# Kernel optimization log

Measured on AMD Instinct MI355X. Metric: run time of the kernel, lower is better.

Reference implementation:

```python
import jax, jax.numpy as jnp
import numpy as np

B, N, D = 8, 4096, 256


def setup_inputs() -> dict:
    key = jax.random.key(0)
    ks = jax.random.split(key, 4)
    seq = jax.random.normal(ks[0], (B, N, D), dtype=jnp.float32)
    W_fts = jax.random.normal(ks[1], (D, D), dtype=jnp.float32) * (1.0 / np.sqrt(D))
    w_f1 = jax.random.normal(ks[2], (D, 1), dtype=jnp.float32) * (1.0 / np.sqrt(D))
    b_f1 = jnp.zeros((1,), dtype=jnp.float32)
    w_f2 = jax.random.normal(ks[3], (D, 1), dtype=jnp.float32) * (1.0 / np.sqrt(D))
    b_f2 = jnp.zeros((1,), dtype=jnp.float32)
    bias = jnp.zeros((1,), dtype=jnp.float32)
    return {"seq": seq, "W_fts": W_fts, "w_f1": w_f1, "b_f1": b_f1,
            "w_f2": w_f2, "b_f2": b_f2, "bias": bias}


def reference(seq, W_fts, w_f1, b_f1, w_f2, b_f2, bias):
    # seq: [B, N, D]
    seq_fts = jnp.einsum('bnd,de->bne', seq, W_fts)          # values, [B, N, D]
    f_1 = seq @ w_f1 + b_f1                                   # [B, N, 1]
    f_2 = seq @ w_f2 + b_f2                                   # [B, N, 1]
    logits = f_1 + jnp.swapaxes(f_2, 1, 2)                    # broadcast add -> [B, N, N]
    coefs = jax.nn.softmax(jax.nn.leaky_relu(logits, negative_slope=0.01), axis=-1)
    vals = jnp.einsum('bnm,bmd->bnd', coefs, seq_fts)         # [B, N, D]
    ret = vals + bias
    return jax.nn.relu(ret)
```

## Files before the change

kernel.cpp:

```cpp
#include <hip/hip_runtime.h>
#include <hip/hip_bf16.h>
#include <math.h>

#define B 8
#define N 4096
#define D 256
#define BN (B*N)
#define NSUP 64
#define NS1 65
#define NR1 4097

typedef __attribute__((ext_vector_type(8))) short bf16x8;
typedef __attribute__((ext_vector_type(4))) float f32x4;

#define GLD16(src, dst) __builtin_amdgcn_global_load_lds( \
    (const __attribute__((address_space(1))) void*)(src), \
    (__attribute__((address_space(3))) void*)(dst), 16, 0, 0)

__device__ __forceinline__ ushort bf16_hi(float x) {
  __hip_bfloat16 h = __float2bfloat16(x);
  return *(ushort*)&h;
}
__device__ __forceinline__ ushort bf16_lo(float x) {
  __hip_bfloat16 h = __float2bfloat16(x);
  float hf = __bfloat162float(h);
  __hip_bfloat16 l = __float2bfloat16(x - hf);
  return *(ushort*)&l;
}

__global__ __launch_bounds__(256) void k_f1f2w(const float* __restrict__ seq,
    const float* __restrict__ w1, const float* __restrict__ b1,
    const float* __restrict__ w2, const float* __restrict__ b2,
    const float* __restrict__ W, float* __restrict__ f1, float* __restrict__ f2,
    int* __restrict__ rank, ushort* __restrict__ W3) {
  if (blockIdx.x >= BN/4) {
    int n = blockIdx.x - BN/4;
    int k = threadIdx.x;
    float x = W[(size_t)k * D + n];
    ushort hu = bf16_hi(x), lu = bf16_lo(x);
    W3[(size_t)n * 768 + k] = hu;
    W3[(size_t)n * 768 + 256 + k] = lu;
    W3[(size_t)n * 768 + 512 + k] = hu;
    return;
  }
  int wave = threadIdx.x >> 6;
  int lane = threadIdx.x & 63;
  long row = (long)blockIdx.x * 4 + wave;
  float4 v = ((const float4*)(seq + row * D))[lane];
  float4 a = ((const float4*)w1)[lane];
  float4 b = ((const float4*)w2)[lane];
  float s1 = v.x*a.x + v.y*a.y + v.z*a.z + v.w*a.w;
  float s2 = v.x*b.x + v.y*b.y + v.z*b.z + v.w*b.w;
  for (int off = 32; off; off >>= 1) {
    s1 += __shfl_xor(s1, off, 64);
    s2 += __shfl_xor(s2, off, 64);
  }
  if (lane == 0) {
    f1[row] = s1 + b1[0];
    f2[row] = s2 + b2[0];
    rank[row] = 0;
  }
}

__global__ __launch_bounds__(256) void k_rank_count(const float* __restrict__ f2,
    int* __restrict__ rank) {
  __shared__ unsigned long long skey[256];
  int b = blockIdx.z;
  int tid = threadIdx.x;
  const float* fb = f2 + (long)b * N;
  int p = blockIdx.y * 256 + tid;
  unsigned int up = __float_as_uint(fb[p]);
  up ^= (unsigned int)(((int)up >> 31) | 0x80000000);
  skey[tid] = ((unsigned long long)up << 12) | (unsigned)p;
  unsigned long long kj[4];
  int jbase = blockIdx.x * 1024;
  #pragma unroll
  for (int q = 0; q < 4; ++q) {
    int j = jbase + q * 256 + tid;
    unsigned int uj = __float_as_uint(fb[j]);
    uj ^= (unsigned int)(((int)uj >> 31) | 0x80000000);
    kj[q] = ((unsigned long long)uj << 12) | (unsigned)j;
  }
  __syncthreads();
  int c[4] = {0, 0, 0, 0};
  const ulonglong2* sk2 = (const ulonglong2*)skey;
  #pragma unroll 4
  for (int pp = 0; pp < 128; ++pp) {
    ulonglong2 kk = sk2[pp];
    #pragma unroll
    for (int q = 0; q < 4; ++q) {
      c[q] += (kk.x < kj[q]) ? 1 : 0;
      c[q] += (kk.y < kj[q]) ? 1 : 0;
    }
  }
  #pragma unroll
  for (int q = 0; q < 4; ++q)
    atomicAdd(&rank[(long)b * N + jbase + q * 256 + tid], c[q]);
}

__global__ __launch_bounds__(256) void k_scatter(const float* __restrict__ f2,
    const int* __restrict__ rank, float* __restrict__ sF2, int* __restrict__ sIdx,
    float* __restrict__ e2lo, float* __restrict__ e2hi) {
  long idx = (long)blockIdx.x * 256 + threadIdx.x;
  int b = (int)(idx >> 12);
  int j = (int)(idx & (N - 1));
  float v = f2[idx];
  int cnt = rank[idx];
  long o = (long)b * N + cnt;
  sF2[o] = v;
  sIdx[o] = j;
  e2lo[o] = expf(0.01f * v);
  e2hi[o] = expf(v);
}

__global__ __launch_bounds__(256) void k_mfma(const float* __restrict__ seq,
    const int* __restrict__ sIdx, const ushort* __restrict__ W3,
    const float* __restrict__ e2lo, const float* __restrict__ e2hi,
    float* __restrict__ Rel, float* __restrict__ Zrel,
    float* __restrict__ SupBaseLo, float* __restrict__ SupBaseHi,
    float* __restrict__ SupZlo, float* __restrict__ SupZhi) {
  __shared__ __align__(16) char smem[64 * 256 * 4];
  ushort (*As)[72] = (ushort(*)[72])smem;
  ushort (*Bs)[64] = (ushort(*)[64])(smem + 64 * 72 * 2);
  int tid = threadIdx.x;
  int wid = tid >> 6, lane = tid & 63;
  int mBase = blockIdx.x * 64;
  int b = mBase >> 12;
  int ar = tid >> 2, aq = tid & 3;
  const float* aSrc = seq + (((size_t)(b << 12)) + sIdx[mBase + ar]) * D + aq * 16;
  int lr = lane >> 3;
  int lcSw = (((lane & 7) ^ (lr & 7))) * 8;
  int wr = wid >> 1, wc = wid & 1, g = lane >> 4, r16 = lane & 15;
  int bswz = r16 & 7;

  f32x4 acc[2][8];
  #pragma unroll
  for (int m = 0; m < 2; ++m)
    #pragma unroll
    for (int n = 0; n < 8; ++n) {
      acc[m][n][0] = 0.f; acc[m][n][1] = 0.f; acc[m][n][2] = 0.f; acc[m][n][3] = 0.f;
    }

  float4 xv[4];
  #pragma unroll
  for (int i = 0; i < 4; ++i) xv[i] = *(const float4*)(aSrc + i * 4);

  for (int kt = 0; kt < 768; kt += 64) {
    ushort ou[16];
    if (kt < 512) {
      #pragma unroll
      for (int i = 0; i < 4; ++i) {
        ou[i*4+0] = bf16_hi(xv[i].x); ou[i*4+1] = bf16_hi(xv[i].y);
        ou[i*4+2] = bf16_hi(xv[i].z); ou[i*4+3] = bf16_hi(xv[i].w);
      }
    } else {
      #pragma unroll
      for (int i = 0; i < 4; ++i) {
        ou[i*4+0] = bf16_lo(xv[i].x); ou[i*4+1] = bf16_lo(xv[i].y);
        ou[i*4+2] = bf16_lo(xv[i].z); ou[i*4+3] = bf16_lo(xv[i].w);
      }
    }
    __syncthreads();
    #pragma unroll
    for (int i = 0; i < 4; ++i)
      *(ushort4*)&As[ar][aq * 16 + i * 4] =
          make_ushort4(ou[i*4+0], ou[i*4+1], ou[i*4+2], ou[i*4+3]);
    #pragma unroll
    for (int q = 0; q < 8; ++q) {
      int r0 = q * 32 + wid * 8;
      GLD16(W3 + (size_t)(r0 + lr) * 768 + kt + lcSw, &Bs[r0][0]);
    }
    if (kt < 704) {
      int nacol = (kt + 64) & 255;
      #pragma unroll
      for (int i = 0; i < 4; ++i) xv[i] = *(const float4*)(aSrc + nacol + i * 4);
    }
    __syncthreads();
    #pragma unroll
    for (int kk = 0; kk < 64; kk += 32) {
      bf16x8 av[2], bv[8];
      #pragma unroll
      for (int m = 0; m < 2; ++m)
        av[m] = *(const bf16x8*)&As[wr*32 + m*16 + r16][kk + g*8];
      int jb = (kk >> 3) + g;
      int jj = jb ^ bswz;
      #pragma unroll
      for (int n = 0; n < 8; ++n) {
        int row = wc*128 + n*16 + r16;
        bv[n] = *(const bf16x8*)((const char*)Bs + row * 128 + jj * 16);
      }
      #pragma unroll
      for (int m = 0; m < 2; ++m)
        #pragma unroll
        for (int n = 0; n < 8; ++n)
          acc[m][n] = __builtin_amdgcn_mfma_f32_16x16x32_bf16(av[m], bv[n], acc[m][n], 0, 0, 0);
    }
  }

  __syncthreads();
  float (*Vt)[256] = (float(*)[256])smem;
  int cswz = (g << 2) | ((g & 1) << 4);
  #pragma unroll
  for (int m = 0; m < 2; ++m)
    #pragma unroll
    for (int n = 0; n < 8; ++n) {
      int col = (wc*128 + n*16 + r16) ^ cswz;
      #pragma unroll
      for (int j = 0; j < 4; ++j)
        Vt[wr*32 + m*16 + g*4 + j][col] = acc[m][n][j];
    }
  __syncthreads();
  int d = tid;
  int s = (mBase >> 6) & 63;
  size_t rb = (size_t)mBase;
  float rl = 0.f, rh = 0.f;
  float* pR = Rel + ((size_t)b * NR1 + (size_t)s * 64) * 512 + 2 * d;
  #pragma unroll 8
  for (int r = 0; r < 64; ++r) {
    int gr = (r >> 2) & 3;
    int rsw = (gr << 2) | ((gr & 1) << 4);
    float wlo = e2lo[rb + r], whi = e2hi[rb + r];
    float v = Vt[r][d ^ rsw];
    float2 pr; pr.x = rl; pr.y = rh;
    *(float2*)(pR + (size_t)r * 512) = pr;
    rl += wlo * v; rh += whi * v;
  }
  SupBaseLo[((size_t)b * NS1 + s) * D + d] = rl;
  SupBaseHi[((size_t)b * NS1 + s) * D + d] = rh;
  if (tid == 0) {
    float z = 0.f;
    #pragma unroll 8
    for (int r = 0; r < 64; ++r) { Zrel[((size_t)b * NR1 + s*64 + r) * 2] = z; z += e2lo[rb + r]; }
    SupZlo[b*NS1+s] = z;
  } else if (tid == 64) {
    float z = 0.f;
    #pragma unroll 8
    for (int r = 0; r < 64; ++r) { Zrel[((size_t)b * NR1 + s*64 + r) * 2 + 1] = z; z += e2hi[rb + r]; }
    SupZhi[b*NS1+s] = z;
  }
}

__global__ __launch_bounds__(256) void k_supscan(float* __restrict__ SupBaseLo,
    float* __restrict__ SupBaseHi, float* __restrict__ SupZlo,
    float* __restrict__ SupZhi, float* __restrict__ Rel, float* __restrict__ Zrel) {
  int b = blockIdx.x, t = threadIdx.x;
  if (t < 64) {
    float4* lo = (float4*)SupBaseLo + (size_t)b * NS1 * 64 + t;
    float4* hi = (float4*)SupBaseHi + (size_t)b * NS1 * 64 + t;
    float4 rl = {0,0,0,0}, rh = {0,0,0,0};
    for (int s = 0; s < NSUP; s += 8) {
      float4 tl[8], th[8];
      #pragma unroll
      for (int u = 0; u < 8; ++u) { tl[u] = lo[(size_t)(s+u)*64]; th[u] = hi[(size_t)(s+u)*64]; }
      #pragma unroll
      for (int u = 0; u < 8; ++u) {
        lo[(size_t)(s+u)*64] = rl; hi[(size_t)(s+u)*64] = rh;
        rl.x+=tl[u].x; rl.y+=tl[u].y; rl.z+=tl[u].z; rl.w+=tl[u].w;
        rh.x+=th[u].x; rh.y+=th[u].y; rh.z+=th[u].z; rh.w+=th[u].w;
      }
    }
    lo[(size_t)NSUP*64] = rl;
    hi[(size_t)NSUP*64] = rh;
  } else if (t < 192) {
    float4 z = {0,0,0,0};
    ((float4*)(Rel + ((size_t)b * NR1 + 4096) * 512))[t - 64] = z;
  } else if (t == 192) {
    float r = 0.f;
    for (int s = 0; s < NSUP; ++s) { float x = SupZlo[b*NS1+s]; SupZlo[b*NS1+s] = r; r += x; }
    SupZlo[b*NS1+NSUP] = r;
    Zrel[((size_t)b * NR1 + 4096) * 2] = 0.f;
  } else if (t == 193) {
    float r = 0.f;
    for (int s = 0; s < NSUP; ++s) { float x = SupZhi[b*NS1+s]; SupZhi[b*NS1+s] = r; r += x; }
    SupZhi[b*NS1+NSUP] = r;
    Zrel[((size_t)b * NR1 + 4096) * 2 + 1] = 0.f;
  }
}

__global__ __launch_bounds__(256) void k_combine2(const float* __restrict__ f1,
    const float* __restrict__ sF2, const float* __restrict__ Rel,
    const float* __restrict__ SupBaseLo, const float* __restrict__ SupBaseHi,
    const float* __restrict__ SupZlo, const float* __restrict__ SupZhi,
    const float* __restrict__ Zrel,
    const float* __restrict__ bias, float* __restrict__ out) {
  int wid = threadIdx.x >> 6, lane = threadIdx.x & 63;
  size_t i = (size_t)blockIdx.x * 4 + wid;
  int b = (int)(i >> 12);
  float f1v = f1[i];
  const float* sb = sF2 + ((size_t)b << 12);
  float t = -f1v;
  int lo = 0, hi = N;
  while (lo < hi) { int mid = (lo + hi) >> 1; if (sb[mid] <= t) lo = mid + 1; else hi = mid; }
  int k = lo;
  int s = k >> 6;
  float a = expf(f1v), cc = expf(0.01f * f1v);
  const float* rrow = Rel + ((size_t)b * NR1 + k) * 512;
  float4 q0 = ((const float4*)rrow)[2*lane];
  float4 q1 = ((const float4*)rrow)[2*lane + 1];
  float4 sblo = ((const float4*)SupBaseLo)[((size_t)b * NS1 + s) * 64 + lane];
  float4 sbhi = ((const float4*)SupBaseHi)[((size_t)b * NS1 + s) * 64 + lane];
  float4 pht  = ((const float4*)SupBaseHi)[((size_t)b * NS1 + NSUP) * 64 + lane];
  float2 z2 = *(const float2*)(Zrel + ((size_t)b * NR1 + k) * 2);
  float Zlo = SupZlo[b*NS1+s] + z2.x;
  float Zhi = SupZhi[b*NS1+NSUP] - SupZhi[b*NS1+s] - z2.y;
  float Z = a * Zhi + cc * Zlo;
  float rz = 1.f / Z;
  float bs = bias[0];
  float4 o4;
  o4.x = fmaxf((a*(pht.x - sbhi.x - q0.y) + cc*(sblo.x + q0.x)) * rz + bs, 0.f);
  o4.y = fmaxf((a*(pht.y - sbhi.y - q0.w) + cc*(sblo.y + q0.z)) * rz + bs, 0.f);
  o4.z = fmaxf((a*(pht.z - sbhi.z - q1.y) + cc*(sblo.z + q1.x)) * rz + bs, 0.f);
  o4.w = fmaxf((a*(pht.w - sbhi.w - q1.w) + cc*(sblo.w + q1.z)) * rz + bs, 0.f);
  ((float4*)out)[i * 64 + lane] = o4;
}

extern "C" void kernel_launch(void* const* d_in, const int* in_sizes, int n_in,
                              void* d_out, int out_size, void* d_ws, size_t ws_size,
                              hipStream_t stream) {
  const float* seq  = (const float*)d_in[0];
  const float* Wf   = (const float*)d_in[1];
  const float* w1   = (const float*)d_in[2];
  const float* b1   = (const float*)d_in[3];
  const float* w2   = (const float*)d_in[4];
  const float* b2   = (const float*)d_in[5];
  const float* bias = (const float*)d_in[6];
  float* out = (float*)d_out;

  size_t needFloats = (size_t)7*BN + (size_t)B*NR1*512 + 2*(size_t)B*NS1*D
                    + 2*(size_t)B*NS1 + 2*(size_t)B*NR1;
  size_t need = needFloats * 4 + (size_t)256 * 768 * 2;
  if (ws_size < need) return;

  float* f1   = (float*)d_ws;
  float* f2   = f1 + BN;
  float* sF2  = f2 + BN;
  float* e2lo = sF2 + BN;
  float* e2hi = e2lo + BN;
  int* sIdx   = (int*)(e2hi + BN);
  int* rank   = sIdx + BN;
  float* Rel  = (float*)(rank + BN);
  float* SupBaseLo = Rel + (size_t)B * NR1 * 512;
  float* SupBaseHi = SupBaseLo + (size_t)B * NS1 * D;
  float* SupZlo = SupBaseHi + (size_t)B * NS1 * D;
  float* SupZhi = SupZlo + B * NS1;
  float* Zrel   = SupZhi + B * NS1;
  ushort* W3 = (ushort*)(Zrel + 2 * (size_t)B * NR1);

  k_f1f2w<<<dim3(BN/4 + 256), 256, 0, stream>>>(seq, w1, b1, w2, b2, Wf,
      f1, f2, rank, W3);
  k_rank_count<<<dim3(N/1024, N/256, B), 256, 0, stream>>>(f2, rank);
  k_scatter<<<dim3(BN/256), 256, 0, stream>>>(f2, rank, sF2, sIdx, e2lo, e2hi);
  k_mfma<<<dim3(BN/64), 256, 0, stream>>>(seq, sIdx, W3, e2lo, e2hi,
      Rel, Zrel, SupBaseLo, SupBaseHi, SupZlo, SupZhi);
  k_supscan<<<dim3(B), 256, 0, stream>>>(SupBaseLo, SupBaseHi, SupZlo, SupZhi,
      Rel, Zrel);
  k_combine2<<<dim3(BN/4), 256, 0, stream>>>(f1, sF2, Rel,
      SupBaseLo, SupBaseHi, SupZlo, SupZhi, Zrel, bias, out);
}
```

Measured before the change: 88.37 us.

## Double-buffer W3 tile in LDS and prefetch seq rows two stages ahead

The single B tile buffer in the projection MFMA kernel becomes two LDS buffers. The next W3 slice is loaded asynchronously with global_load_lds while MFMAs run on the current slice, and the bf16 hi/lo conversion of the next A chunk moves after the compute, with a second register stage prefetching seq two steps ahead. The A tile row pitch also changes from 72 to 76 ushorts, presumably to cut LDS bank conflicts. The aim is to hide global load latency behind compute, at the cost of more LDS, more registers and an extra barrier per iteration. The new pitch is not a multiple of 16 bytes, so 128-bit A reads lose alignment.

```diff
diff --git a/kernel.cpp b/kernel.cpp
--- a/kernel.cpp
+++ b/kernel.cpp
@@ -9,6 +9,7 @@
 #define NSUP 64
 #define NS1 65
 #define NR1 4097
+#define ALD 76
 
 typedef __attribute__((ext_vector_type(8))) short bf16x8;
 typedef __attribute__((ext_vector_type(4))) float f32x4;
@@ -119,9 +120,9 @@
     float* __restrict__ Rel, float* __restrict__ Zrel,
     float* __restrict__ SupBaseLo, float* __restrict__ SupBaseHi,
     float* __restrict__ SupZlo, float* __restrict__ SupZhi) {
-  __shared__ __align__(16) char smem[64 * 256 * 4];
-  ushort (*As)[72] = (ushort(*)[72])smem;
-  ushort (*Bs)[64] = (ushort(*)[64])(smem + 64 * 72 * 2);
+  __shared__ __align__(16) char smem[64*ALD*2 + 2*256*64*2];
+  ushort (*As)[ALD] = (ushort(*)[ALD])smem;
+  ushort (*BsBuf)[64] = (ushort(*)[64])(smem + 64 * ALD * 2);
   int tid = threadIdx.x;
   int wid = tid >> 6, lane = tid & 63;
   int mBase = blockIdx.x * 64;
@@ -141,41 +142,44 @@
       acc[m][n][0] = 0.f; acc[m][n][1] = 0.f; acc[m][n][2] = 0.f; acc[m][n][3] = 0.f;
     }
 
-  float4 xv[4];
-  #pragma unroll
-  for (int i = 0; i < 4; ++i) xv[i] = *(const float4*)(aSrc + i * 4);
+  float4 xvA[4], xvB[4];
+  ushort ou[16];
+  #pragma unroll
+  for (int i = 0; i < 4; ++i) xvA[i] = *(const float4*)(aSrc + i * 4);
+  #pragma unroll
+  for (int i = 0; i < 4; ++i) {
+    ou[i*4+0] = bf16_hi(xvA[i].x); ou[i*4+1] = bf16_hi(xvA[i].y);
+    ou[i*4+2] = bf16_hi(xvA[i].z); ou[i*4+3] = bf16_hi(xvA[i].w);
+  }
+  #pragma unroll
+  for (int q = 0; q < 8; ++q) {
+    int r0 = q * 32 + wid * 8;
+    GLD16(W3 + (size_t)(r0 + lr) * 768 + 0 + lcSw, &BsBuf[r0][0]);
+  }
+  #pragma unroll
+  for (int i = 0; i < 4; ++i) xvA[i] = *(const float4*)(aSrc + 64 + i * 4);
 
   for (int kt = 0; kt < 768; kt += 64) {
-    ushort ou[16];
-    if (kt < 512) {
-      #pragma unroll
-      for (int i = 0; i < 4; ++i) {
-        ou[i*4+0] = bf16_hi(xv[i].x); ou[i*4+1] = bf16_hi(xv[i].y);
-        ou[i*4+2] = bf16_hi(xv[i].z); ou[i*4+3] = bf16_hi(xv[i].w);
-      }
-    } else {
-      #pragma unroll
-      for (int i = 0; i < 4; ++i) {
-        ou[i*4+0] = bf16_lo(xv[i].x); ou[i*4+1] = bf16_lo(xv[i].y);
-        ou[i*4+2] = bf16_lo(xv[i].z); ou[i*4+3] = bf16_lo(xv[i].w);
-      }
-    }
+    int cur = (kt >> 6) & 1;
     __syncthreads();
     #pragma unroll
     for (int i = 0; i < 4; ++i)
       *(ushort4*)&As[ar][aq * 16 + i * 4] =
           make_ushort4(ou[i*4+0], ou[i*4+1], ou[i*4+2], ou[i*4+3]);
-    #pragma unroll
-    for (int q = 0; q < 8; ++q) {
-      int r0 = q * 32 + wid * 8;
-      GLD16(W3 + (size_t)(r0 + lr) * 768 + kt + lcSw, &Bs[r0][0]);
-    }
+    __syncthreads();
     if (kt < 704) {
-      int nacol = (kt + 64) & 255;
-      #pragma unroll
-      for (int i = 0; i < 4; ++i) xv[i] = *(const float4*)(aSrc + nacol + i * 4);
-    }
-    __syncthreads();
+      int nkt = kt + 64;
+      #pragma unroll
+      for (int q = 0; q < 8; ++q) {
+        int r0 = q * 32 + wid * 8;
+        GLD16(W3 + (size_t)(r0 + lr) * 768 + nkt + lcSw, &BsBuf[(cur ^ 1) * 256 + r0][0]);
+      }
+    }
+    if (kt <= 576) {
+      int nacol = (kt + 128) & 255;
+      #pragma unroll
+      for (int i = 0; i < 4; ++i) xvB[i] = *(const float4*)(aSrc + nacol + i * 4);
+    }
     #pragma unroll
     for (int kk = 0; kk < 64; kk += 32) {
       bf16x8 av[2], bv[8];
@@ -186,14 +190,31 @@
       int jj = jb ^ bswz;
       #pragma unroll
       for (int n = 0; n < 8; ++n) {
-        int row = wc*128 + n*16 + r16;
-        bv[n] = *(const bf16x8*)((const char*)Bs + row * 128 + jj * 16);
+        int row = cur * 256 + wc*128 + n*16 + r16;
+        bv[n] = *(const bf16x8*)((const char*)BsBuf + row * 128 + jj * 16);
       }
       #pragma unroll
       for (int m = 0; m < 2; ++m)
         #pragma unroll
         for (int n = 0; n < 8; ++n)
           acc[m][n] = __builtin_amdgcn_mfma_f32_16x16x32_bf16(av[m], bv[n], acc[m][n], 0, 0, 0);
+    }
+    if (kt < 704) {
+      if (kt + 64 < 512) {
+        #pragma unroll
+        for (int i = 0; i < 4; ++i) {
+          ou[i*4+0] = bf16_hi(xvA[i].x); ou[i*4+1] = bf16_hi(xvA[i].y);
+          ou[i*4+2] = bf16_hi(xvA[i].z); ou[i*4+3] = bf16_hi(xvA[i].w);
+        }
+      } else {
+        #pragma unroll
+        for (int i = 0; i < 4; ++i) {
+          ou[i*4+0] = bf16_lo(xvA[i].x); ou[i*4+1] = bf16_lo(xvA[i].y);
+          ou[i*4+2] = bf16_lo(xvA[i].z); ou[i*4+3] = bf16_lo(xvA[i].w);
+        }
+      }
+      #pragma unroll
+      for (int i = 0; i < 4; ++i) xvA[i] = xvB[i];
     }
   }
 
```

After: 92.01 us. +4.1%, slower.
